# Kernel tuning notes

Measured on AMD Instinct MI355X. Metric: run time of the kernel, lower is better.

## Reference

```python
import jax, jax.numpy as jnp
import numpy as np

DIM = 128

def _complex_linear_params(key, dim, scale=0.05):
    k1, k2, k3, k4 = jax.random.split(key, 4)
    Wr = jax.random.normal(k1, (dim, dim), jnp.float32) * scale
    Wi = jax.random.normal(k2, (dim, dim), jnp.float32) * scale
    br = jax.random.normal(k3, (dim,), jnp.float32) * scale
    bi = jax.random.normal(k4, (dim,), jnp.float32) * scale
    return Wr, Wi, br, bi

def setup_inputs() -> dict:
    key = jax.random.key(0)
    ks = jax.random.split(key, 8)
    B, C, Ht, Wt = 8, DIM, 64, 64
    Hs, Ws = 32, 32
    inp = {
        'target_r': jax.random.normal(ks[0], (B, C, Ht, Wt), jnp.float32),
        'target_i': jax.random.normal(ks[1], (B, C, Ht, Wt), jnp.float32),
        'source_r': jax.random.normal(ks[2], (B, C, Hs, Ws), jnp.float32),
        'source_i': jax.random.normal(ks[3], (B, C, Hs, Ws), jnp.float32),
    }
    for name, k in zip(('q', 'k', 'v'), ks[4:7]):
        Wr, Wi, br, bi = _complex_linear_params(k, DIM)
        inp[f'W{name}_r'], inp[f'W{name}_i'] = Wr, Wi
        inp[f'b{name}_r'], inp[f'b{name}_i'] = br, bi
    inp['gamma'] = jnp.float32(0.1)
    return inp

def reference(target_r, target_i, source_r, source_i,
              Wq_r, Wq_i, bq_r, bq_i,
              Wk_r, Wk_i, bk_r, bk_i,
              Wv_r, Wv_i, bv_r, bv_i, gamma):
    B, C, Ht, Wt = target_r.shape
    _, _, Hs, Ws = source_r.shape
    Nt, Ns = Ht * Wt, Hs * Ws
    scale = jnp.float32(C ** 0.5)
    # complex tensors [B, N, C]
    t = (target_r + 1j * target_i).reshape(B, C, Nt).transpose(0, 2, 1)
    s = (source_r + 1j * source_i).reshape(B, C, Ns).transpose(0, 2, 1)
    Wq = Wq_r + 1j * Wq_i; Wk = Wk_r + 1j * Wk_i; Wv = Wv_r + 1j * Wv_i
    Q = jnp.einsum('bnc,dc->bnd', t, Wq) + (bq_r + 1j * bq_i)
    K = jnp.einsum('bmc,dc->bmd', s, Wk) + (bk_r + 1j * bk_i)
    V = jnp.einsum('bmc,dc->bmd', s, Wv) + (bv_r + 1j * bv_i)
    # complex QK^H, keep only real part for softmax
    attn = jnp.einsum('bnd,bmd->bnm', Q, jnp.conj(K))  # [B, Nt, Ns] complex
    w = jax.nn.softmax(attn.real / scale, axis=-1)      # real weights
    out = jnp.einsum('bnm,bmd->bnd', w.astype(V.dtype), V)  # complex [B, Nt, C]
    out = out.transpose(0, 2, 1).reshape(B, C, Ht, Wt)
    return gamma * out
```

## Files before the change

### kernel.cpp

```cpp
#include <hip/hip_runtime.h>
#include <hip/hip_bf16.h>

#define NB 8
#define NC 128
#define NT 4096
#define NS 1024

typedef short bf16x8 __attribute__((ext_vector_type(8)));
typedef float f32x4  __attribute__((ext_vector_type(4)));

#define MFMA16(a, b, c) __builtin_amdgcn_mfma_f32_16x16x32_bf16(a, b, c, 0, 0, 0)

__device__ __forceinline__ short f2b(float x) {
    __hip_bfloat16 h = __float2bfloat16(x);
    return *reinterpret_cast<short*>(&h);
}

__device__ __forceinline__ void gl_lds16(const void* g, void* l) {
    __builtin_amdgcn_global_load_lds(
        (const __attribute__((address_space(1))) unsigned int*)g,
        (__attribute__((address_space(3))) unsigned int*)l, 16, 0, 0);
}

__global__ __launch_bounds__(256) void pack_w_kernel(
    const float* __restrict__ Wqr, const float* __restrict__ Wqi,
    const float* __restrict__ Wkr, const float* __restrict__ Wki,
    const float* __restrict__ Wvr, const float* __restrict__ Wvi,
    __hip_bfloat16* __restrict__ WqT, __hip_bfloat16* __restrict__ WkT,
    __hip_bfloat16* __restrict__ WvT)
{
    const int idx = blockIdx.x * 256 + threadIdx.x;
    const float *Wr, *Wi; __hip_bfloat16* dst; int base;
    if (idx < 65536)       { Wr = Wqr; Wi = Wqi; dst = WqT; base = idx; }
    else if (idx < 131072) { Wr = Wkr; Wi = Wki; dst = WkT; base = idx - 65536; }
    else                   { Wr = Wvr; Wi = Wvi; dst = WvT; base = idx - 131072; }
    const int dp = base >> 8, k = base & 255;
    const int d  = dp & 127;
    float v;
    if (dp < 128) v = (k < 128) ? Wr[d * 128 + k] : -Wi[d * 128 + k - 128];
    else          v = (k < 128) ? Wi[d * 128 + k] :  Wr[d * 128 + k - 128];
    dst[base] = __float2bfloat16(v);
}

__global__ __launch_bounds__(256) void projKV_kernel(
    const float* __restrict__ Xr, const float* __restrict__ Xi,
    const __hip_bfloat16* __restrict__ WkT, const __hip_bfloat16* __restrict__ WvT,
    const float* __restrict__ bkr, const float* __restrict__ bki,
    const float* __restrict__ bvr,
    __hip_bfloat16* __restrict__ Kh, __hip_bfloat16* __restrict__ VrT)
{
    __shared__ __align__(16) char smem[13568];
    const int b   = blockIdx.x & 7;
    const int n0  = (blockIdx.x >> 3) * 16;
    const int tid = threadIdx.x;

    for (int i = tid; i < 16 * 64; i += 256) {
        const int cp = i >> 4, n = i & 15, c = cp * 2;
        const size_t rb = (size_t)(b * NC + c) * NS + n0 + n;
        const unsigned pr = (unsigned short)f2b(Xr[rb]) |
                            ((unsigned)(unsigned short)f2b(Xr[rb + NS]) << 16);
        const unsigned pi = (unsigned short)f2b(Xi[rb]) |
                            ((unsigned)(unsigned short)f2b(Xi[rb + NS]) << 16);
        *(unsigned*)(smem + n * 528 + c * 2)         = pr;
        *(unsigned*)(smem + n * 528 + (128 + c) * 2) = pi;
    }
    __syncthreads();

    const int w = tid >> 6, l15 = tid & 15, q = (tid & 63) >> 4;

    const char* wp[6];
    #pragma unroll
    for (int jj = 0; jj < 6; ++jj) {
        const int j = w * 6 + jj;
        wp[jj] = (j < 16)
            ? (const char*)WkT + (size_t)(j * 16 + l15) * 512 + q * 16
            : (const char*)WvT + (size_t)((j - 16) * 16 + l15) * 512 + q * 16;
    }

    f32x4 acc[6];
    #pragma unroll
    for (int jj = 0; jj < 6; ++jj) { acc[jj][0]=0.f; acc[jj][1]=0.f; acc[jj][2]=0.f; acc[jj][3]=0.f; }

    #pragma unroll
    for (int t = 0; t < 8; ++t) {
        const bf16x8 af = *(const bf16x8*)(smem + l15 * 528 + (t * 32 + q * 8) * 2);
        #pragma unroll
        for (int jj = 0; jj < 6; ++jj) {
            const bf16x8 bf = *(const bf16x8*)(wp[jj] + t * 64);
            acc[jj] = MFMA16(af, bf, acc[jj]);
        }
    }

    #pragma unroll
    for (int jj = 0; jj < 6; ++jj) {
        const int j = w * 6 + jj;
        if (j < 16) {
            const int col = j * 16 + l15;
            const float bv = (col < 128) ? bkr[col] : bki[col - 128];
            #pragma unroll
            for (int r = 0; r < 4; ++r) {
                const int n = n0 + q * 4 + r;
                Kh[((size_t)(b * NS + n) << 8) + col] = __float2bfloat16(acc[jj][r] + bv);
            }
        } else {
            const int d = (j - 16) * 16 + l15;
            #pragma unroll
            for (int r = 0; r < 4; ++r)
                *(__hip_bfloat16*)(smem + 8448 + d * 40 + (q * 4 + r) * 2) =
                    __float2bfloat16(acc[jj][r] + bvr[d]);
        }
    }
    __syncthreads();
    for (int i = tid; i < 128 * 2; i += 256) {
        const int d = i >> 1, seg = i & 1;
        const int4 v = *(const int4*)(smem + 8448 + d * 40 + seg * 16);
        *(int4*)((char*)VrT + ((size_t)(b * NC + d) * NS + n0) * 2 + seg * 16) = v;
    }
}

__device__ __forceinline__ void stage_chunk(const char* Kbase, const char* Vbase,
                                            char* buf, int ch, int w, int lane)
{
    const char* ks = Kbase + (size_t)ch * 16384;
    #pragma unroll
    for (int i = 0; i < 4; ++i) {
        const int ml = w * 8 + i * 2 + (lane >> 5);
        const int gr = ((ml >> 2) & 3) * 8 + ((ml >> 4) << 2) + (ml & 3);
        const int so = gr * 512 + (((lane & 31) ^ (ml & 7)) << 4);
        gl_lds16(ks + so, buf + (w * 4 + i) * 1024);
    }
    const char* vsrc = Vbase + (size_t)ch * 64;
    #pragma unroll
    for (int i = 0; i < 2; ++i) {
        const int d  = (w + i * 4) * 16 + (lane >> 2);
        const int so = d * 2048 + (((lane & 3) ^ ((lane >> 2) & 3)) << 4);
        gl_lds16(vsrc + so, buf + 16384 + (w + i * 4) * 1024);
    }
}

__global__ __launch_bounds__(256, 2) void attn_mfma_kernel(
    const float* __restrict__ tr_g, const float* __restrict__ ti_g,
    const __hip_bfloat16* __restrict__ WqT,
    const float* __restrict__ bqr, const float* __restrict__ bqi,
    const __hip_bfloat16* __restrict__ Kh, const __hip_bfloat16* __restrict__ VrT,
    const float* __restrict__ gamma_p, float* __restrict__ out)
{
    __shared__ __align__(16) char smem[73728];
    char* As = smem;

    const int b    = blockIdx.x & 7;
    const int n0   = (blockIdx.x >> 3) * 64;
    const int tid  = threadIdx.x;
    const int w    = tid >> 6, lane = tid & 63, l15 = tid & 15, q = (tid & 63) >> 4;
    const int row0 = w * 16;

    for (int i = tid; i < 64 * 64; i += 256) {
        const int cp = i >> 6, n = i & 63, c = cp * 2;
        const size_t rb = (size_t)(b * NC + c) * NT + n0 + n;
        const unsigned pr = (unsigned short)f2b(tr_g[rb]) |
                            ((unsigned)(unsigned short)f2b(tr_g[rb + NT]) << 16);
        const unsigned pi = (unsigned short)f2b(ti_g[rb]) |
                            ((unsigned)(unsigned short)f2b(ti_g[rb + NT]) << 16);
        *(unsigned*)(As + n * 528 + c * 2)         = pr;
        *(unsigned*)(As + n * 528 + (128 + c) * 2) = pi;
    }
    __syncthreads();

    bf16x8 qf[8];
    {
        f32x4 qacc[16];
        #pragma unroll
        for (int j = 0; j < 16; ++j) { qacc[j][0]=0.f; qacc[j][1]=0.f; qacc[j][2]=0.f; qacc[j][3]=0.f; }
        #pragma unroll
        for (int t = 0; t < 8; ++t) {
            const bf16x8 af = *(const bf16x8*)(As + (row0 + l15) * 528 + (t * 32 + q * 8) * 2);
            #pragma unroll
            for (int j = 0; j < 16; ++j) {
                const int col = j * 16 + l15;
                const bf16x8 bf = *(const bf16x8*)((const char*)WqT + col * 512 + (t * 32 + q * 8) * 2);
                qacc[j] = MFMA16(af, bf, qacc[j]);
            }
        }
        const float inv_s = 0.12751744f;
        #pragma unroll
        for (int j = 0; j < 16; ++j) {
            const int col  = j * 16 + l15;
            const float bv = (col < 128) ? bqr[col] : bqi[col - 128];
            #pragma unroll
            for (int r = 0; r < 4; ++r) {
                const int row = row0 + q * 4 + r;
                *(__hip_bfloat16*)(As + row * 528 + col * 2) =
                    __float2bfloat16((qacc[j][r] + bv) * inv_s);
            }
        }
        #pragma unroll
        for (int t = 0; t < 8; ++t)
            qf[t] = *(const bf16x8*)(As + (row0 + l15) * 528 + (t * 32 + q * 8) * 2);
    }
    __syncthreads();

    const char* Kbase = (const char*)Kh + ((size_t)(b * NS) << 9);
    const char* Vbase = (const char*)VrT + (size_t)b * NC * NS * 2;
    char* bA = smem;
    char* bB = smem + 24576;
    char* bC = smem + 49152;

    stage_chunk(Kbase, Vbase, bA, 0, w, lane);
    stage_chunk(Kbase, Vbase, bB, 1, w, lane);

    f32x4 oacc[8];
    #pragma unroll
    for (int j = 0; j < 8; ++j) { oacc[j][0]=0.f; oacc[j][1]=0.f; oacc[j][2]=0.f; oacc[j][3]=0.f; }
    f32x4 lacc;
    lacc[0]=0.f; lacc[1]=0.f; lacc[2]=0.f; lacc[3]=0.f;

    bf16x8 onesf;
    {
        const short ob = (l15 == 0) ? (short)0x3F80 : (short)0;
        #pragma unroll
        for (int e = 0; e < 8; ++e) onesf[e] = ob;
    }

    const int e3   = l15 & 7;
    const int qx   = q ^ (e3 & 3);
    const int eh   = e3 >> 2;
    const int vswz = (q ^ (l15 & 3)) << 4;

    #pragma unroll 1
    for (int ch = 0; ch < 32; ++ch) {
        asm volatile("s_waitcnt vmcnt(6)" ::: "memory");
        __builtin_amdgcn_s_barrier();

        const int sch = (ch + 2 < 32) ? ch + 2 : 31;
        stage_chunk(Kbase, Vbase, bC, sch, w, lane);

        f32x4 s0v, s1v;
        s0v[0]=0.f; s0v[1]=0.f; s0v[2]=0.f; s0v[3]=0.f;
        s1v[0]=0.f; s1v[1]=0.f; s1v[2]=0.f; s1v[3]=0.f;
        #pragma unroll
        for (int t = 0; t < 8; ++t) {
            const int tb = ((t ^ eh) << 6) + (qx << 4);
            const bf16x8 k0 = *(const bf16x8*)(bA + l15 * 512 + tb);
            s0v = MFMA16(k0, qf[t], s0v);
            const bf16x8 k1 = *(const bf16x8*)(bA + (16 + l15) * 512 + tb);
            s1v = MFMA16(k1, qf[t], s1v);
        }

        bf16x8 pa;
        #pragma unroll
        for (int r = 0; r < 4; ++r) {
            pa[r]     = f2b(exp2f(s0v[r]));
            pa[4 + r] = f2b(exp2f(s1v[r]));
        }

        lacc = MFMA16(pa, onesf, lacc);
        #pragma unroll
        for (int j = 0; j < 8; ++j) {
            const bf16x8 vf = *(const bf16x8*)(bA + 16384 + (j * 16 + l15) * 64 + vswz);
            oacc[j] = MFMA16(pa, vf, oacc[j]);
        }

        char* t0 = bA; bA = bB; bB = bC; bC = t0;
    }

    __syncthreads();
    float* Of = (float*)smem;
    const float g = gamma_p[0];
    #pragma unroll
    for (int r = 0; r < 4; ++r) {
        const float lr = __shfl(lacc[r], q * 16, 64);
        const float inv_l = g / fmaxf(lr, 1e-30f);
        const int m = row0 + q * 4 + r;
        #pragma unroll
        for (int j = 0; j < 8; ++j)
            Of[(j * 16 + l15) * 65 + m] = oacc[j][r] * inv_l;
    }
    __syncthreads();
    float* ob = out + (size_t)b * NC * NT + n0;
    for (int i = tid; i < 128 * 64; i += 256) {
        const int d = i >> 6, m = i & 63;
        ob[(size_t)d * NT + m] = Of[d * 65 + m];
    }
}

extern "C" void kernel_launch(void* const* d_in, const int* in_sizes, int n_in,
                              void* d_out, int out_size, void* d_ws, size_t ws_size,
                              hipStream_t stream)
{
    const float* target_r = (const float*)d_in[0];
    const float* target_i = (const float*)d_in[1];
    const float* source_r = (const float*)d_in[2];
    const float* source_i = (const float*)d_in[3];
    const float* Wq_r = (const float*)d_in[4];
    const float* Wq_i = (const float*)d_in[5];
    const float* bq_r = (const float*)d_in[6];
    const float* bq_i = (const float*)d_in[7];
    const float* Wk_r = (const float*)d_in[8];
    const float* Wk_i = (const float*)d_in[9];
    const float* bk_r = (const float*)d_in[10];
    const float* bk_i = (const float*)d_in[11];
    const float* Wv_r = (const float*)d_in[12];
    const float* Wv_i = (const float*)d_in[13];
    const float* bv_r = (const float*)d_in[14];
    const float* bv_i = (const float*)d_in[15];
    const float* gamma = (const float*)d_in[16];

    char* ws = (char*)d_ws;
    __hip_bfloat16* Kh  = (__hip_bfloat16*)(ws);
    __hip_bfloat16* VrT = (__hip_bfloat16*)(ws + 4194304);
    __hip_bfloat16* WqT = (__hip_bfloat16*)(ws + 6291456);
    __hip_bfloat16* WkT = (__hip_bfloat16*)(ws + 6422528);
    __hip_bfloat16* WvT = (__hip_bfloat16*)(ws + 6553600);

    pack_w_kernel<<<640, 256, 0, stream>>>(Wq_r, Wq_i, Wk_r, Wk_i, Wv_r, Wv_i,
                                           WqT, WkT, WvT);

    projKV_kernel<<<NB * (NS / 16), 256, 0, stream>>>(
        source_r, source_i, WkT, WvT, bk_r, bk_i, bv_r, Kh, VrT);

    attn_mfma_kernel<<<NB * (NT / 64), 256, 0, stream>>>(
        target_r, target_i, WqT, bq_r, bq_i, Kh, VrT, gamma, (float*)d_out);
}
```

Baseline: 190.6 us.

## Switch attention loop to 32x32 MFMA with split-KV across wave pairs

Replaces the 16x16x32 MFMA inner loop with 32x32x16 MFMAs. Each wave now owns 32 query rows, and the two wave pairs alternate key chunks, with partial outputs and row sums reduced through shared memory at the end. The Q projection is redistributed so each wave computes a column slice for all 64 rows, and the K staging layout is simplified to match the new fragment access. This aims to raise MFMA efficiency and cut LDS fragment reads, at the cost of idle chunks per wave, cross-lane shuffles to re-lay P, and a larger epilogue reduction.

```diff
diff --git a/kernel.cpp b/kernel.cpp
--- a/kernel.cpp
+++ b/kernel.cpp
@@ -8,12 +8,18 @@
 
 typedef short bf16x8 __attribute__((ext_vector_type(8)));
 typedef float f32x4  __attribute__((ext_vector_type(4)));
+typedef float f32x16 __attribute__((ext_vector_type(16)));
 
 #define MFMA16(a, b, c) __builtin_amdgcn_mfma_f32_16x16x32_bf16(a, b, c, 0, 0, 0)
+#define MFMA32(a, b, c) __builtin_amdgcn_mfma_f32_32x32x16_bf16(a, b, c, 0, 0, 0)
 
 __device__ __forceinline__ short f2b(float x) {
     __hip_bfloat16 h = __float2bfloat16(x);
     return *reinterpret_cast<short*>(&h);
+}
+
+__device__ __forceinline__ unsigned pk2(float a, float b) {
+    return (unsigned)(unsigned short)f2b(a) | ((unsigned)(unsigned short)f2b(b) << 16);
 }
 
 __device__ __forceinline__ void gl_lds16(const void* g, void* l) {
@@ -125,8 +131,7 @@
     #pragma unroll
     for (int i = 0; i < 4; ++i) {
         const int ml = w * 8 + i * 2 + (lane >> 5);
-        const int gr = ((ml >> 2) & 3) * 8 + ((ml >> 4) << 2) + (ml & 3);
-        const int so = gr * 512 + (((lane & 31) ^ (ml & 7)) << 4);
+        const int so = ml * 512 + (((lane & 31) ^ (ml & 7)) << 4);
         gl_lds16(ks + so, buf + (w * 4 + i) * 1024);
     }
     const char* vsrc = Vbase + (size_t)ch * 64;
@@ -147,12 +152,15 @@
 {
     __shared__ __align__(16) char smem[73728];
     char* As = smem;
+    char* Qh = smem + 33792;
 
     const int b    = blockIdx.x & 7;
     const int n0   = (blockIdx.x >> 3) * 64;
     const int tid  = threadIdx.x;
-    const int w    = tid >> 6, lane = tid & 63, l15 = tid & 15, q = (tid & 63) >> 4;
-    const int row0 = w * 16;
+    const int w    = tid >> 6, lane = tid & 63;
+    const int l15  = lane & 15, q8 = lane >> 4;
+    const int l31  = lane & 31, hi = lane >> 5;
+    const int w01  = w & 1, wprt = w >> 1;
 
     for (int i = tid; i < 64 * 64; i += 256) {
         const int cp = i >> 6, n = i & 63, c = cp * 2;
@@ -166,37 +174,49 @@
     }
     __syncthreads();
 
-    bf16x8 qf[8];
     {
-        f32x4 qacc[16];
-        #pragma unroll
-        for (int j = 0; j < 16; ++j) { qacc[j][0]=0.f; qacc[j][1]=0.f; qacc[j][2]=0.f; qacc[j][3]=0.f; }
+        f32x4 qacc[4][4];
+        #pragma unroll
+        for (int rg = 0; rg < 4; ++rg)
+            #pragma unroll
+            for (int jj = 0; jj < 4; ++jj) {
+                qacc[rg][jj][0]=0.f; qacc[rg][jj][1]=0.f;
+                qacc[rg][jj][2]=0.f; qacc[rg][jj][3]=0.f;
+            }
         #pragma unroll
         for (int t = 0; t < 8; ++t) {
-            const bf16x8 af = *(const bf16x8*)(As + (row0 + l15) * 528 + (t * 32 + q * 8) * 2);
-            #pragma unroll
-            for (int j = 0; j < 16; ++j) {
-                const int col = j * 16 + l15;
-                const bf16x8 bf = *(const bf16x8*)((const char*)WqT + col * 512 + (t * 32 + q * 8) * 2);
-                qacc[j] = MFMA16(af, bf, qacc[j]);
+            bf16x8 af[4];
+            #pragma unroll
+            for (int rg = 0; rg < 4; ++rg)
+                af[rg] = *(const bf16x8*)(As + (rg * 16 + l15) * 528 + (t * 32 + q8 * 8) * 2);
+            #pragma unroll
+            for (int jj = 0; jj < 4; ++jj) {
+                const int col = (w * 4 + jj) * 16 + l15;
+                const bf16x8 bf = *(const bf16x8*)((const char*)WqT + col * 512 + (t * 32 + q8 * 8) * 2);
+                #pragma unroll
+                for (int rg = 0; rg < 4; ++rg)
+                    qacc[rg][jj] = MFMA16(af[rg], bf, qacc[rg][jj]);
             }
         }
         const float inv_s = 0.12751744f;
         #pragma unroll
-        for (int j = 0; j < 16; ++j) {
-            const int col  = j * 16 + l15;
+        for (int jj = 0; jj < 4; ++jj) {
+            const int col  = (w * 4 + jj) * 16 + l15;
             const float bv = (col < 128) ? bqr[col] : bqi[col - 128];
             #pragma unroll
-            for (int r = 0; r < 4; ++r) {
-                const int row = row0 + q * 4 + r;
-                *(__hip_bfloat16*)(As + row * 528 + col * 2) =
-                    __float2bfloat16((qacc[j][r] + bv) * inv_s);
-            }
-        }
-        #pragma unroll
-        for (int t = 0; t < 8; ++t)
-            qf[t] = *(const bf16x8*)(As + (row0 + l15) * 528 + (t * 32 + q * 8) * 2);
-    }
+            for (int rg = 0; rg < 4; ++rg)
+                #pragma unroll
+                for (int r = 0; r < 4; ++r)
+                    *(__hip_bfloat16*)(Qh + (rg * 16 + q8 * 4 + r) * 528 + col * 2) =
+                        __float2bfloat16((qacc[rg][jj][r] + bv) * inv_s);
+        }
+    }
+    __syncthreads();
+
+    bf16x8 qf[16];
+    #pragma unroll
+    for (int t = 0; t < 16; ++t)
+        qf[t] = *(const bf16x8*)(Qh + (w01 * 32 + l31) * 528 + t * 32 + hi * 16);
     __syncthreads();
 
     const char* Kbase = (const char*)Kh + ((size_t)(b * NS) << 9);
@@ -208,23 +228,18 @@
     stage_chunk(Kbase, Vbase, bA, 0, w, lane);
     stage_chunk(Kbase, Vbase, bB, 1, w, lane);
 
-    f32x4 oacc[8];
-    #pragma unroll
-    for (int j = 0; j < 8; ++j) { oacc[j][0]=0.f; oacc[j][1]=0.f; oacc[j][2]=0.f; oacc[j][3]=0.f; }
-    f32x4 lacc;
-    lacc[0]=0.f; lacc[1]=0.f; lacc[2]=0.f; lacc[3]=0.f;
+    f32x16 oacc[4];
+    #pragma unroll
+    for (int jd = 0; jd < 4; ++jd)
+        #pragma unroll
+        for (int r = 0; r < 16; ++r) oacc[jd][r] = 0.f;
+    f32x16 lacc;
+    #pragma unroll
+    for (int r = 0; r < 16; ++r) lacc[r] = 0.f;
 
     bf16x8 onesf;
-    {
-        const short ob = (l15 == 0) ? (short)0x3F80 : (short)0;
-        #pragma unroll
-        for (int e = 0; e < 8; ++e) onesf[e] = ob;
-    }
-
-    const int e3   = l15 & 7;
-    const int qx   = q ^ (e3 & 3);
-    const int eh   = e3 >> 2;
-    const int vswz = (q ^ (l15 & 3)) << 4;
+    #pragma unroll
+    for (int e = 0; e < 8; ++e) onesf[e] = (short)0x3F80;
 
     #pragma unroll 1
     for (int ch = 0; ch < 32; ++ch) {
@@ -234,52 +249,79 @@
         const int sch = (ch + 2 < 32) ? ch + 2 : 31;
         stage_chunk(Kbase, Vbase, bC, sch, w, lane);
 
-        f32x4 s0v, s1v;
-        s0v[0]=0.f; s0v[1]=0.f; s0v[2]=0.f; s0v[3]=0.f;
-        s1v[0]=0.f; s1v[1]=0.f; s1v[2]=0.f; s1v[3]=0.f;
-        #pragma unroll
-        for (int t = 0; t < 8; ++t) {
-            const int tb = ((t ^ eh) << 6) + (qx << 4);
-            const bf16x8 k0 = *(const bf16x8*)(bA + l15 * 512 + tb);
-            s0v = MFMA16(k0, qf[t], s0v);
-            const bf16x8 k1 = *(const bf16x8*)(bA + (16 + l15) * 512 + tb);
-            s1v = MFMA16(k1, qf[t], s1v);
-        }
-
-        bf16x8 pa;
-        #pragma unroll
-        for (int r = 0; r < 4; ++r) {
-            pa[r]     = f2b(exp2f(s0v[r]));
-            pa[4 + r] = f2b(exp2f(s1v[r]));
-        }
-
-        lacc = MFMA16(pa, onesf, lacc);
-        #pragma unroll
-        for (int j = 0; j < 8; ++j) {
-            const bf16x8 vf = *(const bf16x8*)(bA + 16384 + (j * 16 + l15) * 64 + vswz);
-            oacc[j] = MFMA16(pa, vf, oacc[j]);
+        if ((ch & 1) == wprt) {
+            f32x16 s;
+            #pragma unroll
+            for (int r = 0; r < 16; ++r) s[r] = 0.f;
+            #pragma unroll
+            for (int t = 0; t < 16; ++t) {
+                const bf16x8 kf = *(const bf16x8*)(
+                    bA + l31 * 512 + (((2 * t + hi) ^ (l31 & 7)) << 4));
+                s = MFMA32(kf, qf[t], s);
+            }
+            #pragma unroll
+            for (int r = 0; r < 16; ++r) s[r] = exp2f(s[r]);
+
+            #pragma unroll
+            for (int t2 = 0; t2 < 2; ++t2) {
+                const int o = t2 * 8;
+                const unsigned x0 = pk2(s[o + 0], s[o + 1]);
+                const unsigned x1 = pk2(s[o + 2], s[o + 3]);
+                const unsigned y0 = pk2(s[o + 4], s[o + 5]);
+                const unsigned y1 = pk2(s[o + 6], s[o + 7]);
+                const unsigned xs0 = __shfl_xor(x0, 32);
+                const unsigned xs1 = __shfl_xor(x1, 32);
+                const unsigned ys0 = __shfl_xor(y0, 32);
+                const unsigned ys1 = __shfl_xor(y1, 32);
+                union { unsigned u[4]; bf16x8 v; } pu;
+                pu.u[0] = hi ? ys0 : x0;
+                pu.u[1] = hi ? ys1 : x1;
+                pu.u[2] = hi ? y0  : xs0;
+                pu.u[3] = hi ? y1  : xs1;
+                const bf16x8 paf = pu.v;
+                lacc = MFMA32(paf, onesf, lacc);
+                #pragma unroll
+                for (int jd = 0; jd < 4; ++jd) {
+                    const bf16x8 vf = *(const bf16x8*)(
+                        bA + 16384 + (jd * 32 + l31) * 64 +
+                        (((2 * t2 + hi) ^ (l31 & 3)) << 4));
+                    oacc[jd] = MFMA32(paf, vf, oacc[jd]);
+                }
+            }
         }
 
         char* t0 = bA; bA = bB; bB = bC; bC = t0;
     }
 
     __syncthreads();
-    float* Of = (float*)smem;
-    const float g = gamma_p[0];
-    #pragma unroll
-    for (int r = 0; r < 4; ++r) {
-        const float lr = __shfl(lacc[r], q * 16, 64);
-        const float inv_l = g / fmaxf(lr, 1e-30f);
-        const int m = row0 + q * 4 + r;
-        #pragma unroll
-        for (int j = 0; j < 8; ++j)
-            Of[(j * 16 + l15) * 65 + m] = oacc[j][r] * inv_l;
-    }
-    __syncthreads();
+    float* Ofp = (float*)(smem + wprt * 33280);
+    #pragma unroll
+    for (int jd = 0; jd < 4; ++jd)
+        #pragma unroll
+        for (int r = 0; r < 16; ++r) {
+            const int m = w01 * 32 + (r & 3) + 8 * (r >> 2) + 4 * hi;
+            Ofp[(jd * 32 + l31) * 65 + m] = oacc[jd][r];
+        }
+    float* lf = (float*)(smem + 66560);
+    if (l31 == 0) {
+        #pragma unroll
+        for (int r = 0; r < 16; ++r) {
+            const int m = w01 * 32 + (r & 3) + 8 * (r >> 2) + 4 * hi;
+            lf[wprt * 64 + m] = lacc[r];
+        }
+    }
+    __syncthreads();
+    float* invl = (float*)(smem + 67072);
+    if (tid < 64)
+        invl[tid] = gamma_p[0] / fmaxf(lf[tid] + lf[64 + tid], 1e-30f);
+    __syncthreads();
+
+    const float* Of0 = (const float*)smem;
+    const float* Of1 = (const float*)(smem + 33280);
     float* ob = out + (size_t)b * NC * NT + n0;
     for (int i = tid; i < 128 * 64; i += 256) {
         const int d = i >> 6, m = i & 63;
-        ob[(size_t)d * NT + m] = Of[d * 65 + m];
+        ob[(size_t)d * NT + m] = (Of0[d * 65 + m] + Of1[d * 65 + m]) * invl[m];
     }
 }
 
```

Measured after the change: 186.6 us. -2.1%, faster.
